# Kernel tuning notes

Measured on AMD Instinct MI355X. Metric: run time of the kernel, lower is better.

The kernel has to match this reference:

```python
import jax, jax.numpy as jnp
import numpy as np

B, NQ, NK, DQ, DK, DV, H = 8, 256, 512, 256, 256, 256, 64
NEG = -1e6


def setup_inputs() -> dict:
    key = jax.random.key(0)
    k1, k2, k3, k4, k5, k6, k7 = jax.random.split(key, 7)
    return {
        "queries": jax.random.normal(k1, (B, NQ, DQ), dtype=jnp.float32),
        "keys": jax.random.normal(k2, (B, NK, DK), dtype=jnp.float32),
        "values": jax.random.normal(k3, (B, NK, DV), dtype=jnp.float32),
        "valid_lens": jax.random.randint(k4, (B,), 1, NK + 1),
        "Wq": jax.random.normal(k5, (DQ, H), dtype=jnp.float32) / np.sqrt(DQ),
        "Wk": jax.random.normal(k6, (DK, H), dtype=jnp.float32) / np.sqrt(DK),
        "wv": jax.random.normal(k7, (H,), dtype=jnp.float32) / np.sqrt(H),
    }


def reference(queries, keys, values, valid_lens, Wq, Wk, wv):
    # project: [B,NQ,H], [B,NK,H]
    q = jnp.einsum("bqd,dh->bqh", queries, Wq)
    k = jnp.einsum("bkd,dh->bkh", keys, Wk)
    # additive features: [B,NQ,NK,H] -> tanh -> reduce with w_v -> scores [B,NQ,NK]
    features = jnp.tanh(q[:, :, None, :] + k[:, None, :, :])
    scores = jnp.einsum("bqkh,h->bqk", features, wv)
    # masked softmax over key axis (per-batch valid_lens)
    mask = jnp.arange(NK)[None, None, :] < valid_lens[:, None, None]
    scores = jnp.where(mask, scores, NEG)
    attn = jax.nn.softmax(scores, axis=-1)
    # dropout p=0 (eval) -> identity; weighted sum of values [B,NQ,DV]
    return jnp.einsum("bqk,bkv->bqv", attn, values)
```

## Files before the change

kernel.cpp:

```cpp
#include <hip/hip_runtime.h>
#include <hip/hip_bf16.h>

constexpr int B  = 8;
constexpr int NQ = 256;
constexpr int NK = 512;
constexpr int D  = 256;
constexpr int DV = 256;
constexpr int H  = 64;
constexpr float NEG = -1e6f;
constexpr float LOG2E = 1.4426950408889634f;

constexpr int RPB = 8;

__global__ __launch_bounds__(256) void proj_kernel(
    const float* __restrict__ queries, const float* __restrict__ keys,
    const float* __restrict__ Wq, const float* __restrict__ Wk,
    float* __restrict__ qp, float* __restrict__ kp)
{
    const int r0 = blockIdx.x * RPB;
    const bool isQ = (r0 < B * NQ);
    const float* src = isQ ? queries + (size_t)r0 * D
                           : keys + (size_t)(r0 - B * NQ) * D;
    const float* W   = isQ ? Wq : Wk;
    float* out       = isQ ? qp + (size_t)r0 * H
                           : kp + (size_t)(r0 - B * NQ) * H;

    __shared__ __align__(16) float rows[RPB][D];
#pragma unroll
    for (int j = 0; j < 2; ++j)
        ((float4*)&rows[0][0])[threadIdx.x + j * 256] =
            ((const float4*)src)[threadIdx.x + j * 256];
    __syncthreads();

    const int h = threadIdx.x & 63;
    const int g = threadIdx.x >> 6;
    float s0 = 0.f, s1 = 0.f;
#pragma unroll 2
    for (int d4 = 0; d4 < D / 4; ++d4) {
        float w0 = W[(d4 * 4 + 0) * H + h];
        float w1 = W[(d4 * 4 + 1) * H + h];
        float w2 = W[(d4 * 4 + 2) * H + h];
        float w3 = W[(d4 * 4 + 3) * H + h];
        float4 ra = *(const float4*)&rows[g][d4 * 4];
        float4 rb = *(const float4*)&rows[g + 4][d4 * 4];
        s0 = fmaf(ra.x, w0, s0);  s1 = fmaf(rb.x, w0, s1);
        s0 = fmaf(ra.y, w1, s0);  s1 = fmaf(rb.y, w1, s1);
        s0 = fmaf(ra.z, w2, s0);  s1 = fmaf(rb.z, w2, s1);
        s0 = fmaf(ra.w, w3, s0);  s1 = fmaf(rb.w, w3, s1);
    }
    out[g * H + h]       = s0;
    out[(g + 4) * H + h] = s1;
}

constexpr int KT   = 128;
constexpr int KPAD = 68;

#define FMA4(acc, a, v) \
    acc.x = fmaf(a, v.x, acc.x); acc.y = fmaf(a, v.y, acc.y); \
    acc.z = fmaf(a, v.z, acc.z); acc.w = fmaf(a, v.w, acc.w);

__global__ __launch_bounds__(512, 4) void attn_kernel(
    const float* __restrict__ qp, const float* __restrict__ kp,
    const float* __restrict__ values, const int* __restrict__ valid_lens,
    const float* __restrict__ wv, float* __restrict__ out)
{
    const int b    = blockIdx.x >> 6;
    const int q0   = (blockIdx.x & 63) * 4;
    const int t    = threadIdx.x;
    const int w    = t >> 6;
    const int l    = t & 63;
    const int qloc = w >> 1;
    const int half = w & 1;

    __shared__ __align__(16) float kT[KT * KPAD];
    __shared__ __align__(16) float qv[4][H];
    __shared__ __align__(16) float w2[H];
    __shared__ __align__(16) float sc[4][NK];

    if (half == 0)
        qv[qloc][l] = qp[((size_t)b * NQ + q0 + qloc) * H + l];

    const float wvl = wv[l];
    float swv = wvl;
#pragma unroll
    for (int off = 32; off > 0; off >>= 1) swv += __shfl_xor(swv, off);
    if (w == 0) w2[l] = -2.f * wvl;

    const int vlen = valid_lens[b];

    for (int kt = 0; kt < NK / KT; ++kt) {
        const int kg = kt * KT + half * 64 + l;
        if (kt * KT < vlen) {
            __syncthreads();
            const float* src = kp + ((size_t)b * NK + kt * KT) * H;
#pragma unroll
            for (int j = 0; j < 4; ++j) {
                int idx4 = t + j * 512;
                int kk = idx4 >> 4;
                int hb = (idx4 & 15) * 4;
                float4 v = ((const float4*)src)[idx4];
                *(float4*)&kT[kk * KPAD + hb] = v;
            }
            __syncthreads();

            const float* qrow = &qv[qloc][0];
            const float* krow = &kT[(half * 64 + l) * KPAD];
            float s0 = 0.f;
#pragma unroll
            for (int h4 = 0; h4 < H / 4; ++h4) {
                float4 qq = *(const float4*)&qrow[h4 * 4];
                float4 ww = *(const float4*)&w2[h4 * 4];
                float4 kk = *(const float4*)&krow[h4 * 4];
                const float C = 2.f * LOG2E;
                float r;
                r = __builtin_amdgcn_rcpf(__builtin_amdgcn_exp2f((qq.x + kk.x) * C) + 1.f);
                s0 = fmaf(ww.x, r, s0);
                r = __builtin_amdgcn_rcpf(__builtin_amdgcn_exp2f((qq.y + kk.y) * C) + 1.f);
                s0 = fmaf(ww.y, r, s0);
                r = __builtin_amdgcn_rcpf(__builtin_amdgcn_exp2f((qq.z + kk.z) * C) + 1.f);
                s0 = fmaf(ww.z, r, s0);
                r = __builtin_amdgcn_rcpf(__builtin_amdgcn_exp2f((qq.w + kk.w) * C) + 1.f);
                s0 = fmaf(ww.w, r, s0);
            }
            sc[qloc][kg] = (kg < vlen) ? (s0 + swv) : NEG;
        } else {
            sc[qloc][kg] = NEG;
        }
    }
    __syncthreads();

    float vals[8];
    float m = -INFINITY;
#pragma unroll
    for (int j = 0; j < 8; ++j) {
        vals[j] = sc[qloc][l + j * 64];
        m = fmaxf(m, vals[j]);
    }
#pragma unroll
    for (int off = 32; off > 0; off >>= 1) m = fmaxf(m, __shfl_xor(m, off));
    float sum = 0.f;
#pragma unroll
    for (int j = 0; j < 8; ++j) {
        float p = __builtin_amdgcn_exp2f((vals[j] - m) * LOG2E);
        vals[j] = p;
        sum += p;
    }
#pragma unroll
    for (int off = 32; off > 0; off >>= 1) sum += __shfl_xor(sum, off);
    const float rinv = __builtin_amdgcn_rcpf(sum);
    if (half == 0) {
        sc[qloc][l + 0 * 64] = vals[0] * rinv;
        sc[qloc][l + 1 * 64] = vals[1] * rinv;
        sc[qloc][l + 2 * 64] = vals[2] * rinv;
        sc[qloc][l + 3 * 64] = vals[3] * rinv;
    } else {
        sc[qloc][l + 4 * 64] = vals[4] * rinv;
        sc[qloc][l + 5 * 64] = vals[5] * rinv;
        sc[qloc][l + 6 * 64] = vals[6] * rinv;
        sc[qloc][l + 7 * 64] = vals[7] * rinv;
    }
    __syncthreads();

    float4 acc0 = {0,0,0,0}, acc1 = {0,0,0,0}, acc2 = {0,0,0,0}, acc3 = {0,0,0,0};
    const float* Vb = values + (size_t)b * NK * DV;
    const int kbeg = w * 64;
    const int kend = min(vlen - kbeg, 64);
    const int kcnt = (kend > 0) ? ((kend + 3) >> 2) : 0;
    for (int c = 0; c < kcnt; ++c) {
        const int k = kbeg + 4 * c;
        float4 a0 = *(const float4*)&sc[0][k];
        float4 a1 = *(const float4*)&sc[1][k];
        float4 a2 = *(const float4*)&sc[2][k];
        float4 a3 = *(const float4*)&sc[3][k];
        const float* vr = Vb + (size_t)k * DV + 4 * l;
        float4 v0 = *(const float4*)(vr);
        float4 v1 = *(const float4*)(vr + DV);
        float4 v2 = *(const float4*)(vr + 2 * DV);
        float4 v3 = *(const float4*)(vr + 3 * DV);
        FMA4(acc0, a0.x, v0); FMA4(acc0, a0.y, v1); FMA4(acc0, a0.z, v2); FMA4(acc0, a0.w, v3);
        FMA4(acc1, a1.x, v0); FMA4(acc1, a1.y, v1); FMA4(acc1, a1.z, v2); FMA4(acc1, a1.w, v3);
        FMA4(acc2, a2.x, v0); FMA4(acc2, a2.y, v1); FMA4(acc2, a2.z, v2); FMA4(acc2, a2.w, v3);
        FMA4(acc3, a3.x, v0); FMA4(acc3, a3.y, v1); FMA4(acc3, a3.z, v2); FMA4(acc3, a3.w, v3);
    }

    float* pt = kT;
    *(float4*)&pt[(w * 4 + 0) * 256 + 4 * l] = acc0;
    *(float4*)&pt[(w * 4 + 1) * 256 + 4 * l] = acc1;
    *(float4*)&pt[(w * 4 + 2) * 256 + 4 * l] = acc2;
    *(float4*)&pt[(w * 4 + 3) * 256 + 4 * l] = acc3;
    __syncthreads();

    if (w < 4) {
        float4 r = {0,0,0,0};
#pragma unroll
        for (int s = 0; s < 8; ++s) {
            float4 p = *(const float4*)&pt[(s * 4 + w) * 256 + 4 * l];
            r.x += p.x; r.y += p.y; r.z += p.z; r.w += p.w;
        }
        *(float4*)&out[((size_t)b * NQ + q0 + w) * DV + 4 * l] = r;
    }
}

extern "C" void kernel_launch(void* const* d_in, const int* in_sizes, int n_in,
                              void* d_out, int out_size, void* d_ws, size_t ws_size,
                              hipStream_t stream) {
    const float* queries    = (const float*)d_in[0];
    const float* keys       = (const float*)d_in[1];
    const float* values     = (const float*)d_in[2];
    const int*   valid_lens = (const int*)d_in[3];
    const float* Wq         = (const float*)d_in[4];
    const float* Wk         = (const float*)d_in[5];
    const float* wv         = (const float*)d_in[6];
    float* out = (float*)d_out;

    float* qp = (float*)d_ws;
    float* kp = qp + (size_t)B * NQ * H;

    proj_kernel<<<(B * NQ + B * NK) / RPB, 256, 0, stream>>>(
        queries, keys, Wq, Wk, qp, kp);

    attn_kernel<<<B * (NQ / 4), 512, 0, stream>>>(
        qp, kp, values, valid_lens, wv, out);
}
```

Baseline: 105.5 us.

## Fold tanh scale into projection, interleave batches, rebalance PV loop

The projection kernel now handles 16 rows per block and multiplies its outputs by 2*log2(e), so the attention inner loop no longer does that multiply per element. Attention blocks are reordered so consecutive blocks belong to different batches, spreading uneven valid lengths across the GPU. The PV accumulation now strides 4-key chunks round-robin over the 8 waves instead of giving each wave a fixed 64-key range, which balances work when vlen is short. The costs are fewer proj blocks with more registers each, and a different summation order.

```diff
diff --git a/kernel.cpp b/kernel.cpp
--- a/kernel.cpp
+++ b/kernel.cpp
@@ -9,8 +9,9 @@
 constexpr int H  = 64;
 constexpr float NEG = -1e6f;
 constexpr float LOG2E = 1.4426950408889634f;
-
-constexpr int RPB = 8;
+constexpr float CSCALE = 2.f * LOG2E;
+
+constexpr int RPB = 16;
 
 __global__ __launch_bounds__(256) void proj_kernel(
     const float* __restrict__ queries, const float* __restrict__ keys,
@@ -27,14 +28,14 @@
 
     __shared__ __align__(16) float rows[RPB][D];
 #pragma unroll
-    for (int j = 0; j < 2; ++j)
+    for (int j = 0; j < 4; ++j)
         ((float4*)&rows[0][0])[threadIdx.x + j * 256] =
             ((const float4*)src)[threadIdx.x + j * 256];
     __syncthreads();
 
     const int h = threadIdx.x & 63;
     const int g = threadIdx.x >> 6;
-    float s0 = 0.f, s1 = 0.f;
+    float s0 = 0.f, s1 = 0.f, s2 = 0.f, s3 = 0.f;
 #pragma unroll 2
     for (int d4 = 0; d4 < D / 4; ++d4) {
         float w0 = W[(d4 * 4 + 0) * H + h];
@@ -43,13 +44,21 @@
         float w3 = W[(d4 * 4 + 3) * H + h];
         float4 ra = *(const float4*)&rows[g][d4 * 4];
         float4 rb = *(const float4*)&rows[g + 4][d4 * 4];
+        float4 rc = *(const float4*)&rows[g + 8][d4 * 4];
+        float4 rd = *(const float4*)&rows[g + 12][d4 * 4];
         s0 = fmaf(ra.x, w0, s0);  s1 = fmaf(rb.x, w0, s1);
+        s2 = fmaf(rc.x, w0, s2);  s3 = fmaf(rd.x, w0, s3);
         s0 = fmaf(ra.y, w1, s0);  s1 = fmaf(rb.y, w1, s1);
+        s2 = fmaf(rc.y, w1, s2);  s3 = fmaf(rd.y, w1, s3);
         s0 = fmaf(ra.z, w2, s0);  s1 = fmaf(rb.z, w2, s1);
+        s2 = fmaf(rc.z, w2, s2);  s3 = fmaf(rd.z, w2, s3);
         s0 = fmaf(ra.w, w3, s0);  s1 = fmaf(rb.w, w3, s1);
-    }
-    out[g * H + h]       = s0;
-    out[(g + 4) * H + h] = s1;
+        s2 = fmaf(rc.w, w3, s2);  s3 = fmaf(rd.w, w3, s3);
+    }
+    out[g * H + h]        = s0 * CSCALE;
+    out[(g + 4) * H + h]  = s1 * CSCALE;
+    out[(g + 8) * H + h]  = s2 * CSCALE;
+    out[(g + 12) * H + h] = s3 * CSCALE;
 }
 
 constexpr int KT   = 128;
@@ -64,8 +73,8 @@
     const float* __restrict__ values, const int* __restrict__ valid_lens,
     const float* __restrict__ wv, float* __restrict__ out)
 {
-    const int b    = blockIdx.x >> 6;
-    const int q0   = (blockIdx.x & 63) * 4;
+    const int b    = blockIdx.x & 7;
+    const int q0   = (blockIdx.x >> 3) * 4;
     const int t    = threadIdx.x;
     const int w    = t >> 6;
     const int l    = t & 63;
@@ -111,15 +120,14 @@
                 float4 qq = *(const float4*)&qrow[h4 * 4];
                 float4 ww = *(const float4*)&w2[h4 * 4];
                 float4 kk = *(const float4*)&krow[h4 * 4];
-                const float C = 2.f * LOG2E;
                 float r;
-                r = __builtin_amdgcn_rcpf(__builtin_amdgcn_exp2f((qq.x + kk.x) * C) + 1.f);
+                r = __builtin_amdgcn_rcpf(__builtin_amdgcn_exp2f(qq.x + kk.x) + 1.f);
                 s0 = fmaf(ww.x, r, s0);
-                r = __builtin_amdgcn_rcpf(__builtin_amdgcn_exp2f((qq.y + kk.y) * C) + 1.f);
+                r = __builtin_amdgcn_rcpf(__builtin_amdgcn_exp2f(qq.y + kk.y) + 1.f);
                 s0 = fmaf(ww.y, r, s0);
-                r = __builtin_amdgcn_rcpf(__builtin_amdgcn_exp2f((qq.z + kk.z) * C) + 1.f);
+                r = __builtin_amdgcn_rcpf(__builtin_amdgcn_exp2f(qq.z + kk.z) + 1.f);
                 s0 = fmaf(ww.z, r, s0);
-                r = __builtin_amdgcn_rcpf(__builtin_amdgcn_exp2f((qq.w + kk.w) * C) + 1.f);
+                r = __builtin_amdgcn_rcpf(__builtin_amdgcn_exp2f(qq.w + kk.w) + 1.f);
                 s0 = fmaf(ww.w, r, s0);
             }
             sc[qloc][kg] = (kg < vlen) ? (s0 + swv) : NEG;
@@ -163,11 +171,9 @@
 
     float4 acc0 = {0,0,0,0}, acc1 = {0,0,0,0}, acc2 = {0,0,0,0}, acc3 = {0,0,0,0};
     const float* Vb = values + (size_t)b * NK * DV;
-    const int kbeg = w * 64;
-    const int kend = min(vlen - kbeg, 64);
-    const int kcnt = (kend > 0) ? ((kend + 3) >> 2) : 0;
-    for (int c = 0; c < kcnt; ++c) {
-        const int k = kbeg + 4 * c;
+    const int nchunks = (vlen + 3) >> 2;
+    for (int c = w; c < nchunks; c += 8) {
+        const int k = 4 * c;
         float4 a0 = *(const float4*)&sc[0][k];
         float4 a1 = *(const float4*)&sc[1][k];
         float4 a2 = *(const float4*)&sc[2][k];
```

Measured after the change: 102.7 us. -2.6%, faster.
